# Optimization experiments

Measured on AMD Instinct MI355X. Metric: run time of the kernel, lower is better.

Reference implementation:

```python
import jax, jax.numpy as jnp
import numpy as np

B, D, HID, NB = 131072, 64, 256, 8
TAIL = 3.0
MIN_W = MIN_H = MIN_D = 1e-3
TR_IDX = np.arange(0, D, 2)  # mask > 0 -> transformed features (even indices)
ID_IDX = np.arange(1, D, 2)  # mask <= 0 -> identity features (odd indices)
DT = len(TR_IDX)


def _resnet(x, w_in, b_in, blocks, w_out, b_out):
    # nflows ResidualNet: initial linear, pre-activation residual blocks, final linear
    h = x @ w_in.T + b_in
    for (w0, b0, w1, b1) in blocks:
        t = jax.nn.relu(h)
        t = t @ w0.T + b0
        t = jax.nn.relu(t)
        t = t @ w1.T + b1
        h = h + t
    return h @ w_out.T + b_out


def _rq_spline(x, uw, uh, ud):
    # unconstrained rational-quadratic spline with linear tails (nflows)
    const = float(np.log(np.expm1(1.0 - MIN_D)))  # so softplus(const)+MIN_D == 1 at boundaries
    ud = jnp.pad(ud, ((0, 0), (0, 0), (1, 1)), constant_values=const)  # [B, DT, NB+1]
    inside = (x >= -TAIL) & (x <= TAIL)
    xc = jnp.clip(x, -TAIL, TAIL)

    widths = MIN_W + (1.0 - MIN_W * NB) * jax.nn.softmax(uw, axis=-1)
    cumw = jnp.pad(jnp.cumsum(widths, -1), ((0, 0), (0, 0), (1, 0)))
    cumw = 2.0 * TAIL * cumw - TAIL
    cumw = cumw.at[..., 0].set(-TAIL).at[..., -1].set(TAIL)
    widths = cumw[..., 1:] - cumw[..., :-1]

    heights = MIN_H + (1.0 - MIN_H * NB) * jax.nn.softmax(uh, axis=-1)
    cumh = jnp.pad(jnp.cumsum(heights, -1), ((0, 0), (0, 0), (1, 0)))
    cumh = 2.0 * TAIL * cumh - TAIL
    cumh = cumh.at[..., 0].set(-TAIL).at[..., -1].set(TAIL)
    heights = cumh[..., 1:] - cumh[..., :-1]

    deriv = MIN_D + jax.nn.softplus(ud)  # [B, DT, NB+1]

    # per-element bin search over cumulative widths
    idx = jnp.clip(jnp.sum((xc[..., None] >= cumw).astype(jnp.int32), -1) - 1, 0, NB - 1)[..., None]
    g = lambda t: jnp.take_along_axis(t, idx, axis=-1)[..., 0]

    in_cw, in_w = g(cumw[..., :-1]), g(widths)
    in_ch, in_h = g(cumh[..., :-1]), g(heights)
    in_delta = g(heights / widths)
    in_d, in_dp1 = g(deriv[..., :-1]), g(deriv[..., 1:])

    theta = (xc - in_cw) / in_w
    tom = theta * (1.0 - theta)
    num = in_h * (in_delta * theta * theta + in_d * tom)
    den = in_delta + (in_d + in_dp1 - 2.0 * in_delta) * tom
    y = in_ch + num / den
    dnum = in_delta * in_delta * (in_dp1 * theta * theta + 2.0 * in_delta * tom + in_d * (1.0 - theta) ** 2)
    lad = jnp.log(dnum) - 2.0 * jnp.log(den)
    return jnp.where(inside, y, x), jnp.where(inside, lad, 0.0)


def setup_inputs() -> dict:
    key = jax.random.key(0)
    ks = jax.random.split(key, 7)
    s_in = 1.0 / np.sqrt(DT)
    s_h = 1.0 / np.sqrt(HID)
    return {
        "inputs": jax.random.normal(ks[0], (B, D), jnp.float32),
        "w_in": jax.random.normal(ks[1], (HID, DT), jnp.float32) * s_in,
        "b_in": jnp.zeros((HID,), jnp.float32),
        "w0a": jax.random.normal(ks[2], (HID, HID), jnp.float32) * s_h,
        "b0a": jnp.zeros((HID,), jnp.float32),
        "w1a": jax.random.normal(ks[3], (HID, HID), jnp.float32) * s_h,
        "b1a": jnp.zeros((HID,), jnp.float32),
        "w0b": jax.random.normal(ks[4], (HID, HID), jnp.float32) * s_h,
        "b0b": jnp.zeros((HID,), jnp.float32),
        "w1b": jax.random.normal(ks[5], (HID, HID), jnp.float32) * s_h,
        "b1b": jnp.zeros((HID,), jnp.float32),
        "w_out": jax.random.normal(ks[6], (DT * (3 * NB - 1), HID), jnp.float32) * s_h,
        "b_out": jnp.zeros((DT * (3 * NB - 1),), jnp.float32),
    }


def reference(inputs, w_in, b_in, w0a, b0a, w1a, b1a, w0b, b0b, w1b, b1b, w_out, b_out):
    ident = inputs[:, ID_IDX]   # [B, DT]
    trans = inputs[:, TR_IDX]   # [B, DT]
    params = _resnet(ident, w_in, b_in, [(w0a, b0a, w1a, b1a), (w0b, b0b, w1b, b1b)], w_out, b_out)
    params = params.reshape(inputs.shape[0], DT, 3 * NB - 1)
    scale = 1.0 / np.sqrt(HID)  # module scales widths/heights by sqrt(hidden_features)
    uw = params[..., :NB] * scale
    uh = params[..., NB:2 * NB] * scale
    ud = params[..., 2 * NB:]
    y, lad = _rq_spline(trans, uw, uh, ud)
    out = jnp.zeros_like(inputs).at[:, ID_IDX].set(ident).at[:, TR_IDX].set(y)
    return out, jnp.sum(lad, axis=1)  # sum_except_batch
```

## Files before the change

### kernel.cpp

```cpp
#include <hip/hip_runtime.h>
#include <hip/hip_bf16.h>

#define B_TOTAL 131072
#define TS 264
#define PS 193

typedef short short8v __attribute__((ext_vector_type(8)));
typedef float f32x4 __attribute__((ext_vector_type(4)));

__device__ __forceinline__ unsigned short f2bf(float f) {
  union { float f; unsigned u; } v; v.f = f;
  unsigned r = v.u + 0x7FFFu + ((v.u >> 16) & 1u);
  return (unsigned short)(r >> 16);
}

__device__ __forceinline__ unsigned short f2bf_hw(float f) {
  __hip_bfloat16 h = __float2bfloat16(f);
  return *reinterpret_cast<unsigned short*>(&h);
}

__device__ __forceinline__ float frcp(float x) { return __builtin_amdgcn_rcpf(x); }

#define W_IN_OFF   0
#define W0A_OFF    8192
#define W1A_OFF    73728
#define W0B_OFF    139264
#define W1B_OFF    204800
#define WOUT_OFF   270336
#define WS_ELEMS   466944

__global__ void prep_weights(const float* __restrict__ w_in,
                             const float* __restrict__ w0a,
                             const float* __restrict__ w1a,
                             const float* __restrict__ w0b,
                             const float* __restrict__ w1b,
                             const float* __restrict__ w_out,
                             unsigned short* __restrict__ ws) {
  int idx = blockIdx.x * 256 + threadIdx.x;
  if (idx >= WS_ELEMS) return;
  float v;
  if (idx < W0A_OFF)       v = w_in[idx];
  else if (idx < W1A_OFF)  v = w0a[idx - W0A_OFF];
  else if (idx < W0B_OFF)  v = w1a[idx - W1A_OFF];
  else if (idx < W1B_OFF)  v = w0b[idx - W0B_OFF];
  else if (idx < WOUT_OFF) v = w1b[idx - W1B_OFF];
  else {
    int p = idx - WOUT_OFF;
    int row = p >> 8, k = p & 255;
    int dim = row / 24, j = row - dim * 24;
    v = (j < 23) ? w_out[(dim * 23 + j) * 256 + k] : 0.f;
  }
  ws[idx] = f2bf(v);
}

__global__ __launch_bounds__(256, 2)
void fused_main(const float* __restrict__ inp,
                const float* __restrict__ b_in,
                const float* __restrict__ b0a, const float* __restrict__ b1a,
                const float* __restrict__ b0b, const float* __restrict__ b1b,
                const float* __restrict__ b_out,
                const unsigned short* __restrict__ ws,
                float* __restrict__ outp) {
  __shared__ unsigned short Xs[64 * TS];
  __shared__ unsigned short Ys[64 * TS];

  const int tid  = threadIdx.x;
  const int lane = tid & 63;
  const int wave = tid >> 6;
  const int l15  = lane & 15;
  const int lhi  = lane >> 4;
  const int row0 = blockIdx.x * 64;

  const f32x4 zero4 = {0.f, 0.f, 0.f, 0.f};

  f32x4 hreg[4][4];

  {
#pragma unroll
    for (int mi = 0; mi < 4; mi++)
#pragma unroll
      for (int ni = 0; ni < 4; ni++) hreg[mi][ni] = zero4;

    short8v a[4];
#pragma unroll
    for (int mi = 0; mi < 4; mi++) {
      int rg = row0 + mi * 16 + l15;
      const float2* s2 = (const float2*)(inp + (long)rg * 64) + lhi * 8;
#pragma unroll
      for (int i = 0; i < 8; i++)
        a[mi][i] = (short)f2bf_hw(s2[i].y);
    }
    short8v b[4];
#pragma unroll
    for (int ni = 0; ni < 4; ni++) {
      int col = wave * 64 + ni * 16 + l15;
      b[ni] = *(const short8v*)(ws + W_IN_OFF + col * 32 + lhi * 8);
    }
#pragma unroll
    for (int mi = 0; mi < 4; mi++)
#pragma unroll
      for (int ni = 0; ni < 4; ni++)
        hreg[mi][ni] = __builtin_amdgcn_mfma_f32_16x16x32_bf16(a[mi], b[ni], hreg[mi][ni], 0, 0, 0);

#pragma unroll
    for (int ni = 0; ni < 4; ni++) {
      int col = wave * 64 + ni * 16 + l15;
      float bias = b_in[col];
#pragma unroll
      for (int mi = 0; mi < 4; mi++)
#pragma unroll
        for (int r = 0; r < 4; r++) {
          hreg[mi][ni][r] += bias;
          int rl = mi * 16 + lhi * 4 + r;
          Xs[rl * TS + col] = f2bf_hw(fmaxf(hreg[mi][ni][r], 0.f));
        }
    }
  }
  __syncthreads();

#pragma unroll
  for (int blk = 0; blk < 2; ++blk) {
    const unsigned short* wAp = ws + (blk == 0 ? W0A_OFF : W0B_OFF);
    const unsigned short* wBp = ws + (blk == 0 ? W1A_OFF : W1B_OFF);
    const float* bAp = (blk == 0) ? b0a : b0b;
    const float* bBp = (blk == 0) ? b1a : b1b;

    {
      f32x4 acc[4][4];
#pragma unroll
      for (int mi = 0; mi < 4; mi++)
#pragma unroll
        for (int ni = 0; ni < 4; ni++) acc[mi][ni] = zero4;

      for (int kk = 0; kk < 8; ++kk) {
        int kb = kk * 32 + lhi * 8;
        short8v a[4];
#pragma unroll
        for (int mi = 0; mi < 4; mi++)
          a[mi] = *(const short8v*)&Xs[(mi * 16 + l15) * TS + kb];
        short8v b[4];
#pragma unroll
        for (int ni = 0; ni < 4; ni++) {
          int col = wave * 64 + ni * 16 + l15;
          b[ni] = *(const short8v*)(wAp + col * 256 + kb);
        }
#pragma unroll
        for (int mi = 0; mi < 4; mi++)
#pragma unroll
          for (int ni = 0; ni < 4; ni++)
            acc[mi][ni] = __builtin_amdgcn_mfma_f32_16x16x32_bf16(a[mi], b[ni], acc[mi][ni], 0, 0, 0);
      }
#pragma unroll
      for (int ni = 0; ni < 4; ni++) {
        int col = wave * 64 + ni * 16 + l15;
        float bias = bAp[col];
#pragma unroll
        for (int mi = 0; mi < 4; mi++)
#pragma unroll
          for (int r = 0; r < 4; r++) {
            int rl = mi * 16 + lhi * 4 + r;
            Ys[rl * TS + col] = f2bf_hw(fmaxf(acc[mi][ni][r] + bias, 0.f));
          }
      }
    }
    __syncthreads();

    {
      f32x4 acc[4][4];
#pragma unroll
      for (int mi = 0; mi < 4; mi++)
#pragma unroll
        for (int ni = 0; ni < 4; ni++) acc[mi][ni] = zero4;

      for (int kk = 0; kk < 8; ++kk) {
        int kb = kk * 32 + lhi * 8;
        short8v a[4];
#pragma unroll
        for (int mi = 0; mi < 4; mi++)
          a[mi] = *(const short8v*)&Ys[(mi * 16 + l15) * TS + kb];
        short8v b[4];
#pragma unroll
        for (int ni = 0; ni < 4; ni++) {
          int col = wave * 64 + ni * 16 + l15;
          b[ni] = *(const short8v*)(wBp + col * 256 + kb);
        }
#pragma unroll
        for (int mi = 0; mi < 4; mi++)
#pragma unroll
          for (int ni = 0; ni < 4; ni++)
            acc[mi][ni] = __builtin_amdgcn_mfma_f32_16x16x32_bf16(a[mi], b[ni], acc[mi][ni], 0, 0, 0);
      }
#pragma unroll
      for (int ni = 0; ni < 4; ni++) {
        int col = wave * 64 + ni * 16 + l15;
        float bias = bBp[col];
#pragma unroll
        for (int mi = 0; mi < 4; mi++)
#pragma unroll
          for (int r = 0; r < 4; r++) {
            hreg[mi][ni][r] += acc[mi][ni][r] + bias;
            float hv = hreg[mi][ni][r];
            int rl = mi * 16 + lhi * 4 + r;
            Xs[rl * TS + col] = f2bf_hw(blk == 0 ? fmaxf(hv, 0.f) : hv);
          }
      }
    }
    __syncthreads();
  }

  float* p_lds = reinterpret_cast<float*>(Ys);

  float lad0 = 0.f, lad1 = 0.f;
  const int dl  = tid & 7;
  const int rsp = tid >> 3;

  for (int chunk = 0; chunk < 4; ++chunk) {
    f32x4 acc[4][3];
#pragma unroll
    for (int mi = 0; mi < 4; mi++)
#pragma unroll
      for (int ni = 0; ni < 3; ni++) acc[mi][ni] = zero4;

    for (int kk = 0; kk < 8; ++kk) {
      int kb = kk * 32 + lhi * 8;
      short8v a[4];
#pragma unroll
      for (int mi = 0; mi < 4; mi++)
        a[mi] = *(const short8v*)&Xs[(mi * 16 + l15) * TS + kb];
      short8v b[3];
#pragma unroll
      for (int ni = 0; ni < 3; ni++) {
        int col = chunk * 192 + wave * 48 + ni * 16 + l15;
        b[ni] = *(const short8v*)(ws + WOUT_OFF + col * 256 + kb);
      }
#pragma unroll
      for (int mi = 0; mi < 4; mi++)
#pragma unroll
        for (int ni = 0; ni < 3; ni++)
          acc[mi][ni] = __builtin_amdgcn_mfma_f32_16x16x32_bf16(a[mi], b[ni], acc[mi][ni], 0, 0, 0);
    }

#pragma unroll
    for (int half = 0; half < 2; ++half) {
#pragma unroll
      for (int ni = 0; ni < 3; ni++) {
        int cl = wave * 48 + ni * 16 + l15;
        int cg = chunk * 192 + cl;
        int dim = cg / 24;
        int j = cg - dim * 24;
        float bias = (j < 23) ? b_out[dim * 23 + j] : 0.f;
#pragma unroll
        for (int mi2 = 0; mi2 < 2; mi2++)
#pragma unroll
          for (int r = 0; r < 4; r++) {
            int rl = mi2 * 16 + lhi * 4 + r;
            if (j < 23)
              p_lds[rl * PS + cl] = acc[half * 2 + mi2][ni][r] + bias;
          }
      }
      __syncthreads();

      {
        const float S = 0.0625f;
        int dg = chunk * 8 + dl;
        int rg = row0 + half * 32 + rsp;
        const float* pb = &p_lds[rsp * PS + dl * 24];

        float2 xin = *(const float2*)(inp + (long)rg * 64 + 2 * dg);
        float x = xin.x, idv = xin.y;

        float pw[8], ph[8];
#pragma unroll
        for (int i = 0; i < 8; i++) { pw[i] = pb[i] * S; ph[i] = pb[8 + i] * S; }
        float mw = pw[0], mh = ph[0];
#pragma unroll
        for (int i = 1; i < 8; i++) { mw = fmaxf(mw, pw[i]); mh = fmaxf(mh, ph[i]); }
        float ew[8], eh[8], sw = 0.f, sh = 0.f;
#pragma unroll
        for (int i = 0; i < 8; i++) {
          ew[i] = __expf(pw[i] - mw); sw += ew[i];
          eh[i] = __expf(ph[i] - mh); sh += eh[i];
        }
        float invw = 0.992f * frcp(sw), invh = 0.992f * frcp(sh);

        float dv[9];
        dv[0] = 1.f; dv[8] = 1.f;
#pragma unroll
        for (int i = 1; i < 8; i++) {
          float u = pb[16 + i - 1];
          float sp = (u > 15.f) ? u : __logf(1.f + __expf(u));
          dv[i] = 0.001f + sp;
        }

        bool inside = (x >= -3.f) && (x <= 3.f);
        float xc = fminf(3.f, fmaxf(-3.f, x));

        float elo = -3.f, flo = -3.f, cw = 0.f, ch = 0.f;
        float in_cw = -3.f, in_w = 1.f, in_ch = -3.f, in_h = 1.f, in_d = 1.f, in_dp1 = 1.f;
#pragma unroll
        for (int i = 0; i < 8; i++) {
          float wi = 0.001f + ew[i] * invw; cw += wi;
          float hi = 0.001f + eh[i] * invh; ch += hi;
          float ehi = (i == 7) ? 3.f : 6.f * cw - 3.f;
          float fhi = (i == 7) ? 3.f : 6.f * ch - 3.f;
          bool take = (i == 0) || (xc >= elo);
          if (take) {
            in_cw = elo; in_w = ehi - elo;
            in_ch = flo; in_h = fhi - flo;
            in_d = dv[i]; in_dp1 = dv[i + 1];
          }
          elo = ehi; flo = fhi;
        }

        float rw   = frcp(in_w);
        float th   = (xc - in_cw) * rw;
        float omt  = 1.f - th;
        float tom  = th * omt;
        float delta = in_h * rw;
        float num  = in_h * (delta * th * th + in_d * tom);
        float den  = delta + (in_d + in_dp1 - 2.f * delta) * tom;
        float y    = in_ch + num * frcp(den);
        float dnum = delta * delta * (in_dp1 * th * th + 2.f * delta * tom + in_d * omt * omt);
        float lad  = __logf(dnum) - 2.f * __logf(den);

        float yout = inside ? y : x;
        float ladv = inside ? lad : 0.f;

        float2 o; o.x = yout; o.y = idv;
        *(float2*)(outp + (long)rg * 64 + 2 * dg) = o;

        if (half == 0) lad0 += ladv; else lad1 += ladv;
      }
      __syncthreads();
    }
  }

#pragma unroll
  for (int off = 1; off < 8; off <<= 1) {
    lad0 += __shfl_xor(lad0, off);
    lad1 += __shfl_xor(lad1, off);
  }
  if (dl == 0) {
    outp[(long)B_TOTAL * 64 + row0 + rsp]      = lad0;
    outp[(long)B_TOTAL * 64 + row0 + 32 + rsp] = lad1;
  }
}

extern "C" void kernel_launch(void* const* d_in, const int* in_sizes, int n_in,
                              void* d_out, int out_size, void* d_ws, size_t ws_size,
                              hipStream_t stream) {
  const float* inputs = (const float*)d_in[0];
  const float* w_in   = (const float*)d_in[1];
  const float* b_in   = (const float*)d_in[2];
  const float* w0a    = (const float*)d_in[3];
  const float* b0a    = (const float*)d_in[4];
  const float* w1a    = (const float*)d_in[5];
  const float* b1a    = (const float*)d_in[6];
  const float* w0b    = (const float*)d_in[7];
  const float* b0b    = (const float*)d_in[8];
  const float* w1b    = (const float*)d_in[9];
  const float* b1b    = (const float*)d_in[10];
  const float* w_out  = (const float*)d_in[11];
  const float* b_out  = (const float*)d_in[12];
  unsigned short* ws  = (unsigned short*)d_ws;
  float* outp = (float*)d_out;

  prep_weights<<<dim3((WS_ELEMS + 255) / 256), dim3(256), 0, stream>>>(
      w_in, w0a, w1a, w0b, w1b, w_out, ws);
  fused_main<<<dim3(2048), dim3(256), 0, stream>>>(
      inputs, b_in, b0a, b1a, b0b, b1b, b_out, ws, outp);
}
```

Baseline: 390.7 us.

## Swizzle LDS activation layout and software-pipeline GEMM operand loads

Replaces the padded row stride of 264 in the LDS activation tiles with an XOR-swizzled 256-wide layout, which is meant to avoid bank conflicts while trimming LDS use. It also moves the GEMM k-loops into helpers that fully unroll and prefetch operands: global weight fragments are loaded two steps ahead in a triple buffer, and LDS A fragments one step ahead in a double buffer. The goal is to hide global and LDS load latency behind the MFMA work. The extra buffering raises VGPR pressure under launch_bounds(256,2), which could cause spills or lower occupancy.

```diff
diff --git a/kernel.cpp b/kernel.cpp
--- a/kernel.cpp
+++ b/kernel.cpp
@@ -2,7 +2,6 @@
 #include <hip/hip_bf16.h>
 
 #define B_TOTAL 131072
-#define TS 264
 #define PS 193
 
 typedef short short8v __attribute__((ext_vector_type(8)));
@@ -20,6 +19,10 @@
 }
 
 __device__ __forceinline__ float frcp(float x) { return __builtin_amdgcn_rcpf(x); }
+
+__device__ __forceinline__ int swz(int row, int col) {
+  return row * 256 + (((col >> 3) ^ (row & 7)) << 3) + (col & 7);
+}
 
 #define W_IN_OFF   0
 #define W0A_OFF    8192
@@ -53,6 +56,68 @@
   ws[idx] = f2bf(v);
 }
 
+__device__ __forceinline__ void lda4(short8v a[4], const unsigned short* S,
+                                     int l15, int lhi, int kk) {
+  const int su = ((kk * 4 + lhi) ^ (l15 & 7)) << 3;
+#pragma unroll
+  for (int mi = 0; mi < 4; mi++)
+    a[mi] = *(const short8v*)&S[(mi * 16 + l15) * 256 + su];
+}
+
+__device__ __forceinline__ void ldb4(short8v b[4], const unsigned short* __restrict__ wP,
+                                     int cb, int l15, int lhi, int kk) {
+#pragma unroll
+  for (int ni = 0; ni < 4; ni++)
+    b[ni] = *(const short8v*)(wP + (cb + ni * 16 + l15) * 256 + kk * 32 + lhi * 8);
+}
+
+__device__ __forceinline__ void ldb3(short8v b[3], const unsigned short* __restrict__ wP,
+                                     int cb, int l15, int lhi, int kk) {
+#pragma unroll
+  for (int ni = 0; ni < 3; ni++)
+    b[ni] = *(const short8v*)(wP + (cb + ni * 16 + l15) * 256 + kk * 32 + lhi * 8);
+}
+
+__device__ __forceinline__ void mm4(f32x4 acc[4][4], const unsigned short* S,
+                                    const unsigned short* __restrict__ wP,
+                                    int cb, int l15, int lhi) {
+  short8v a[2][4], b[3][4];
+  lda4(a[0], S, l15, lhi, 0);
+  ldb4(b[0], wP, cb, l15, lhi, 0);
+  ldb4(b[1], wP, cb, l15, lhi, 1);
+#pragma unroll
+  for (int kk = 0; kk < 8; ++kk) {
+    if (kk < 6) ldb4(b[(kk + 2) % 3], wP, cb, l15, lhi, kk + 2);
+    if (kk < 7) lda4(a[(kk + 1) & 1], S, l15, lhi, kk + 1);
+#pragma unroll
+    for (int mi = 0; mi < 4; mi++)
+#pragma unroll
+      for (int ni = 0; ni < 4; ni++)
+        acc[mi][ni] = __builtin_amdgcn_mfma_f32_16x16x32_bf16(
+            a[kk & 1][mi], b[kk % 3][ni], acc[mi][ni], 0, 0, 0);
+  }
+}
+
+__device__ __forceinline__ void mm3(f32x4 acc[4][3], const unsigned short* S,
+                                    const unsigned short* __restrict__ wP,
+                                    int cb, int l15, int lhi) {
+  short8v a[2][4], b[3][3];
+  lda4(a[0], S, l15, lhi, 0);
+  ldb3(b[0], wP, cb, l15, lhi, 0);
+  ldb3(b[1], wP, cb, l15, lhi, 1);
+#pragma unroll
+  for (int kk = 0; kk < 8; ++kk) {
+    if (kk < 6) ldb3(b[(kk + 2) % 3], wP, cb, l15, lhi, kk + 2);
+    if (kk < 7) lda4(a[(kk + 1) & 1], S, l15, lhi, kk + 1);
+#pragma unroll
+    for (int mi = 0; mi < 4; mi++)
+#pragma unroll
+      for (int ni = 0; ni < 3; ni++)
+        acc[mi][ni] = __builtin_amdgcn_mfma_f32_16x16x32_bf16(
+            a[kk & 1][mi], b[kk % 3][ni], acc[mi][ni], 0, 0, 0);
+  }
+}
+
 __global__ __launch_bounds__(256, 2)
 void fused_main(const float* __restrict__ inp,
                 const float* __restrict__ b_in,
@@ -61,8 +126,8 @@
                 const float* __restrict__ b_out,
                 const unsigned short* __restrict__ ws,
                 float* __restrict__ outp) {
-  __shared__ unsigned short Xs[64 * TS];
-  __shared__ unsigned short Ys[64 * TS];
+  __shared__ unsigned short Xs[64 * 256];
+  __shared__ unsigned short Ys[64 * 256];
 
   const int tid  = threadIdx.x;
   const int lane = tid & 63;
@@ -112,7 +177,7 @@
         for (int r = 0; r < 4; r++) {
           hreg[mi][ni][r] += bias;
           int rl = mi * 16 + lhi * 4 + r;
-          Xs[rl * TS + col] = f2bf_hw(fmaxf(hreg[mi][ni][r], 0.f));
+          Xs[swz(rl, col)] = f2bf_hw(fmaxf(hreg[mi][ni][r], 0.f));
         }
     }
   }
@@ -132,24 +197,8 @@
 #pragma unroll
         for (int ni = 0; ni < 4; ni++) acc[mi][ni] = zero4;
 
-      for (int kk = 0; kk < 8; ++kk) {
-        int kb = kk * 32 + lhi * 8;
-        short8v a[4];
-#pragma unroll
-        for (int mi = 0; mi < 4; mi++)
-          a[mi] = *(const short8v*)&Xs[(mi * 16 + l15) * TS + kb];
-        short8v b[4];
-#pragma unroll
-        for (int ni = 0; ni < 4; ni++) {
-          int col = wave * 64 + ni * 16 + l15;
-          b[ni] = *(const short8v*)(wAp + col * 256 + kb);
-        }
-#pragma unroll
-        for (int mi = 0; mi < 4; mi++)
-#pragma unroll
-          for (int ni = 0; ni < 4; ni++)
-            acc[mi][ni] = __builtin_amdgcn_mfma_f32_16x16x32_bf16(a[mi], b[ni], acc[mi][ni], 0, 0, 0);
-      }
+      mm4(acc, Xs, wAp, wave * 64, l15, lhi);
+
 #pragma unroll
       for (int ni = 0; ni < 4; ni++) {
         int col = wave * 64 + ni * 16 + l15;
@@ -159,7 +208,7 @@
 #pragma unroll
           for (int r = 0; r < 4; r++) {
             int rl = mi * 16 + lhi * 4 + r;
-            Ys[rl * TS + col] = f2bf_hw(fmaxf(acc[mi][ni][r] + bias, 0.f));
+            Ys[swz(rl, col)] = f2bf_hw(fmaxf(acc[mi][ni][r] + bias, 0.f));
           }
       }
     }
@@ -172,24 +221,8 @@
 #pragma unroll
         for (int ni = 0; ni < 4; ni++) acc[mi][ni] = zero4;
 
-      for (int kk = 0; kk < 8; ++kk) {
-        int kb = kk * 32 + lhi * 8;
-        short8v a[4];
-#pragma unroll
-        for (int mi = 0; mi < 4; mi++)
-          a[mi] = *(const short8v*)&Ys[(mi * 16 + l15) * TS + kb];
-        short8v b[4];
-#pragma unroll
-        for (int ni = 0; ni < 4; ni++) {
-          int col = wave * 64 + ni * 16 + l15;
-          b[ni] = *(const short8v*)(wBp + col * 256 + kb);
-        }
-#pragma unroll
-        for (int mi = 0; mi < 4; mi++)
-#pragma unroll
-          for (int ni = 0; ni < 4; ni++)
-            acc[mi][ni] = __builtin_amdgcn_mfma_f32_16x16x32_bf16(a[mi], b[ni], acc[mi][ni], 0, 0, 0);
-      }
+      mm4(acc, Ys, wBp, wave * 64, l15, lhi);
+
 #pragma unroll
       for (int ni = 0; ni < 4; ni++) {
         int col = wave * 64 + ni * 16 + l15;
@@ -201,7 +234,7 @@
             hreg[mi][ni][r] += acc[mi][ni][r] + bias;
             float hv = hreg[mi][ni][r];
             int rl = mi * 16 + lhi * 4 + r;
-            Xs[rl * TS + col] = f2bf_hw(blk == 0 ? fmaxf(hv, 0.f) : hv);
+            Xs[swz(rl, col)] = f2bf_hw(blk == 0 ? fmaxf(hv, 0.f) : hv);
           }
       }
     }
@@ -221,24 +254,7 @@
 #pragma unroll
       for (int ni = 0; ni < 3; ni++) acc[mi][ni] = zero4;
 
-    for (int kk = 0; kk < 8; ++kk) {
-      int kb = kk * 32 + lhi * 8;
-      short8v a[4];
-#pragma unroll
-      for (int mi = 0; mi < 4; mi++)
-        a[mi] = *(const short8v*)&Xs[(mi * 16 + l15) * TS + kb];
-      short8v b[3];
-#pragma unroll
-      for (int ni = 0; ni < 3; ni++) {
-        int col = chunk * 192 + wave * 48 + ni * 16 + l15;
-        b[ni] = *(const short8v*)(ws + WOUT_OFF + col * 256 + kb);
-      }
-#pragma unroll
-      for (int mi = 0; mi < 4; mi++)
-#pragma unroll
-        for (int ni = 0; ni < 3; ni++)
-          acc[mi][ni] = __builtin_amdgcn_mfma_f32_16x16x32_bf16(a[mi], b[ni], acc[mi][ni], 0, 0, 0);
-    }
+    mm3(acc, Xs, ws + WOUT_OFF, chunk * 192 + wave * 48, l15, lhi);
 
 #pragma unroll
     for (int half = 0; half < 2; ++half) {
```

Result: no change. 397.9 us (+1.9%).

## Cut LDS footprint with swizzled single buffer and per-wave bf16 param staging

Applied to the files above, without the earlier changes.

The padded double activation buffers become a single XOR-swizzled 64x256 bf16 buffer, with extra barriers so it can be reused in place. Output-layer parameters are staged per wave in bf16 rather than in a shared fp32 tile, so the spline stage needs no block-wide barriers. The log-det reduction now runs through a small LDS array. The smaller LDS use allows raising the launch bound to 3 blocks per CU for more occupancy, but risks register spills and loses precision on the spline parameters.

```diff
diff --git a/kernel.cpp b/kernel.cpp
--- a/kernel.cpp
+++ b/kernel.cpp
@@ -2,8 +2,6 @@
 #include <hip/hip_bf16.h>
 
 #define B_TOTAL 131072
-#define TS 264
-#define PS 193
 
 typedef short short8v __attribute__((ext_vector_type(8)));
 typedef float f32x4 __attribute__((ext_vector_type(4)));
@@ -19,7 +17,15 @@
   return *reinterpret_cast<unsigned short*>(&h);
 }
 
+__device__ __forceinline__ float bf2f(unsigned short u) {
+  union { unsigned u; float f; } v; v.u = ((unsigned)u) << 16; return v.f;
+}
+
 __device__ __forceinline__ float frcp(float x) { return __builtin_amdgcn_rcpf(x); }
+
+__device__ __forceinline__ int swz(int row, int col) {
+  return row * 256 + (((col >> 3) ^ (row & 7)) << 3) + (col & 7);
+}
 
 #define W_IN_OFF   0
 #define W0A_OFF    8192
@@ -53,7 +59,7 @@
   ws[idx] = f2bf(v);
 }
 
-__global__ __launch_bounds__(256, 2)
+__global__ __launch_bounds__(256, 3)
 void fused_main(const float* __restrict__ inp,
                 const float* __restrict__ b_in,
                 const float* __restrict__ b0a, const float* __restrict__ b1a,
@@ -61,8 +67,9 @@
                 const float* __restrict__ b_out,
                 const unsigned short* __restrict__ ws,
                 float* __restrict__ outp) {
-  __shared__ unsigned short Xs[64 * TS];
-  __shared__ unsigned short Ys[64 * TS];
+  __shared__ unsigned short Xs[64 * 256];
+  __shared__ unsigned short Pstage[4 * 1536];
+  __shared__ float Red[256];
 
   const int tid  = threadIdx.x;
   const int lane = tid & 63;
@@ -112,7 +119,7 @@
         for (int r = 0; r < 4; r++) {
           hreg[mi][ni][r] += bias;
           int rl = mi * 16 + lhi * 4 + r;
-          Xs[rl * TS + col] = f2bf_hw(fmaxf(hreg[mi][ni][r], 0.f));
+          Xs[swz(rl, col)] = f2bf_hw(fmaxf(hreg[mi][ni][r], 0.f));
         }
     }
   }
@@ -133,23 +140,21 @@
         for (int ni = 0; ni < 4; ni++) acc[mi][ni] = zero4;
 
       for (int kk = 0; kk < 8; ++kk) {
-        int kb = kk * 32 + lhi * 8;
-        short8v a[4];
-#pragma unroll
-        for (int mi = 0; mi < 4; mi++)
-          a[mi] = *(const short8v*)&Xs[(mi * 16 + l15) * TS + kb];
-        short8v b[4];
-#pragma unroll
-        for (int ni = 0; ni < 4; ni++) {
-          int col = wave * 64 + ni * 16 + l15;
-          b[ni] = *(const short8v*)(wAp + col * 256 + kb);
-        }
+        const int su = ((kk * 4 + lhi) ^ (l15 & 7)) << 3;
+        short8v a[4], b[4];
+#pragma unroll
+        for (int mi = 0; mi < 4; mi++)
+          a[mi] = *(const short8v*)&Xs[(mi * 16 + l15) * 256 + su];
+#pragma unroll
+        for (int ni = 0; ni < 4; ni++)
+          b[ni] = *(const short8v*)(wAp + (wave * 64 + ni * 16 + l15) * 256 + kk * 32 + lhi * 8);
 #pragma unroll
         for (int mi = 0; mi < 4; mi++)
 #pragma unroll
           for (int ni = 0; ni < 4; ni++)
             acc[mi][ni] = __builtin_amdgcn_mfma_f32_16x16x32_bf16(a[mi], b[ni], acc[mi][ni], 0, 0, 0);
       }
+      __syncthreads();
 #pragma unroll
       for (int ni = 0; ni < 4; ni++) {
         int col = wave * 64 + ni * 16 + l15;
@@ -159,11 +164,11 @@
 #pragma unroll
           for (int r = 0; r < 4; r++) {
             int rl = mi * 16 + lhi * 4 + r;
-            Ys[rl * TS + col] = f2bf_hw(fmaxf(acc[mi][ni][r] + bias, 0.f));
+            Xs[swz(rl, col)] = f2bf_hw(fmaxf(acc[mi][ni][r] + bias, 0.f));
           }
       }
-    }
-    __syncthreads();
+      __syncthreads();
+    }
 
     {
       f32x4 acc[4][4];
@@ -173,23 +178,21 @@
         for (int ni = 0; ni < 4; ni++) acc[mi][ni] = zero4;
 
       for (int kk = 0; kk < 8; ++kk) {
-        int kb = kk * 32 + lhi * 8;
-        short8v a[4];
-#pragma unroll
-        for (int mi = 0; mi < 4; mi++)
-          a[mi] = *(const short8v*)&Ys[(mi * 16 + l15) * TS + kb];
-        short8v b[4];
-#pragma unroll
-        for (int ni = 0; ni < 4; ni++) {
-          int col = wave * 64 + ni * 16 + l15;
-          b[ni] = *(const short8v*)(wBp + col * 256 + kb);
-        }
+        const int su = ((kk * 4 + lhi) ^ (l15 & 7)) << 3;
+        short8v a[4], b[4];
+#pragma unroll
+        for (int mi = 0; mi < 4; mi++)
+          a[mi] = *(const short8v*)&Xs[(mi * 16 + l15) * 256 + su];
+#pragma unroll
+        for (int ni = 0; ni < 4; ni++)
+          b[ni] = *(const short8v*)(wBp + (wave * 64 + ni * 16 + l15) * 256 + kk * 32 + lhi * 8);
 #pragma unroll
         for (int mi = 0; mi < 4; mi++)
 #pragma unroll
           for (int ni = 0; ni < 4; ni++)
             acc[mi][ni] = __builtin_amdgcn_mfma_f32_16x16x32_bf16(a[mi], b[ni], acc[mi][ni], 0, 0, 0);
       }
+      __syncthreads();
 #pragma unroll
       for (int ni = 0; ni < 4; ni++) {
         int col = wave * 64 + ni * 16 + l15;
@@ -201,18 +204,17 @@
             hreg[mi][ni][r] += acc[mi][ni][r] + bias;
             float hv = hreg[mi][ni][r];
             int rl = mi * 16 + lhi * 4 + r;
-            Xs[rl * TS + col] = f2bf_hw(blk == 0 ? fmaxf(hv, 0.f) : hv);
+            Xs[swz(rl, col)] = f2bf_hw(blk == 0 ? fmaxf(hv, 0.f) : hv);
           }
       }
-    }
-    __syncthreads();
-  }
-
-  float* p_lds = reinterpret_cast<float*>(Ys);
+      __syncthreads();
+    }
+  }
 
   float lad0 = 0.f, lad1 = 0.f;
-  const int dl  = tid & 7;
-  const int rsp = tid >> 3;
+  const int dsl = lane >> 5;
+  const int rsp = lane & 31;
+  unsigned short* Pw = &Pstage[wave * 1536];
 
   for (int chunk = 0; chunk < 4; ++chunk) {
     f32x4 acc[4][3];
@@ -222,16 +224,15 @@
       for (int ni = 0; ni < 3; ni++) acc[mi][ni] = zero4;
 
     for (int kk = 0; kk < 8; ++kk) {
-      int kb = kk * 32 + lhi * 8;
-      short8v a[4];
-#pragma unroll
-      for (int mi = 0; mi < 4; mi++)
-        a[mi] = *(const short8v*)&Xs[(mi * 16 + l15) * TS + kb];
-      short8v b[3];
+      const int su = ((kk * 4 + lhi) ^ (l15 & 7)) << 3;
+      short8v a[4], b[3];
+#pragma unroll
+      for (int mi = 0; mi < 4; mi++)
+        a[mi] = *(const short8v*)&Xs[(mi * 16 + l15) * 256 + su];
 #pragma unroll
       for (int ni = 0; ni < 3; ni++) {
         int col = chunk * 192 + wave * 48 + ni * 16 + l15;
-        b[ni] = *(const short8v*)(ws + WOUT_OFF + col * 256 + kb);
+        b[ni] = *(const short8v*)(ws + WOUT_OFF + col * 256 + kk * 32 + lhi * 8);
       }
 #pragma unroll
       for (int mi = 0; mi < 4; mi++)
@@ -241,37 +242,46 @@
     }
 
 #pragma unroll
-    for (int half = 0; half < 2; ++half) {
+    for (int hf = 0; hf < 2; ++hf) {
 #pragma unroll
       for (int ni = 0; ni < 3; ni++) {
-        int cl = wave * 48 + ni * 16 + l15;
-        int cg = chunk * 192 + cl;
-        int dim = cg / 24;
-        int j = cg - dim * 24;
+        int cl = ni * 16 + l15;
+        int ds = (cl >= 24) ? 1 : 0;
+        int j  = cl - ds * 24;
+        int dim = chunk * 8 + wave * 2 + ds;
         float bias = (j < 23) ? b_out[dim * 23 + j] : 0.f;
 #pragma unroll
         for (int mi2 = 0; mi2 < 2; mi2++)
 #pragma unroll
           for (int r = 0; r < 4; r++) {
-            int rl = mi2 * 16 + lhi * 4 + r;
+            int row = mi2 * 16 + lhi * 4 + r;
             if (j < 23)
-              p_lds[rl * PS + cl] = acc[half * 2 + mi2][ni][r] + bias;
+              Pw[ds * 768 + row * 24 + j] = f2bf_hw(acc[hf * 2 + mi2][ni][r] + bias);
           }
       }
-      __syncthreads();
 
       {
         const float S = 0.0625f;
-        int dg = chunk * 8 + dl;
-        int rg = row0 + half * 32 + rsp;
-        const float* pb = &p_lds[rsp * PS + dl * 24];
+        int dg = chunk * 8 + wave * 2 + dsl;
+        int rg = row0 + hf * 32 + rsp;
+        const unsigned short* pb16 = &Pw[dsl * 768 + rsp * 24];
+        short8v pv0 = *(const short8v*)(pb16);
+        short8v pv1 = *(const short8v*)(pb16 + 8);
+        short8v pv2 = *(const short8v*)(pb16 + 16);
+        float pf[24];
+#pragma unroll
+        for (int i = 0; i < 8; i++) {
+          pf[i]      = bf2f((unsigned short)pv0[i]);
+          pf[8 + i]  = bf2f((unsigned short)pv1[i]);
+          pf[16 + i] = bf2f((unsigned short)pv2[i]);
+        }
 
         float2 xin = *(const float2*)(inp + (long)rg * 64 + 2 * dg);
         float x = xin.x, idv = xin.y;
 
         float pw[8], ph[8];
 #pragma unroll
-        for (int i = 0; i < 8; i++) { pw[i] = pb[i] * S; ph[i] = pb[8 + i] * S; }
+        for (int i = 0; i < 8; i++) { pw[i] = pf[i] * S; ph[i] = pf[8 + i] * S; }
         float mw = pw[0], mh = ph[0];
 #pragma unroll
         for (int i = 1; i < 8; i++) { mw = fmaxf(mw, pw[i]); mh = fmaxf(mh, ph[i]); }
@@ -287,7 +297,7 @@
         dv[0] = 1.f; dv[8] = 1.f;
 #pragma unroll
         for (int i = 1; i < 8; i++) {
-          float u = pb[16 + i - 1];
+          float u = pf[16 + i - 1];
           float sp = (u > 15.f) ? u : __logf(1.f + __expf(u));
           dv[i] = 0.001f + sp;
         }
@@ -329,20 +339,21 @@
         float2 o; o.x = yout; o.y = idv;
         *(float2*)(outp + (long)rg * 64 + 2 * dg) = o;
 
-        if (half == 0) lad0 += ladv; else lad1 += ladv;
-      }
-      __syncthreads();
-    }
-  }
-
-#pragma unroll
-  for (int off = 1; off < 8; off <<= 1) {
-    lad0 += __shfl_xor(lad0, off);
-    lad1 += __shfl_xor(lad1, off);
-  }
-  if (dl == 0) {
-    outp[(long)B_TOTAL * 64 + row0 + rsp]      = lad0;
-    outp[(long)B_TOTAL * 64 + row0 + 32 + rsp] = lad1;
+        if (hf == 0) lad0 += ladv; else lad1 += ladv;
+      }
+    }
+  }
+
+  lad0 += __shfl_xor(lad0, 32);
+  lad1 += __shfl_xor(lad1, 32);
+  if (lane < 32) {
+    Red[wave * 64 + lane]      = lad0;
+    Red[wave * 64 + 32 + lane] = lad1;
+  }
+  __syncthreads();
+  if (tid < 64) {
+    float s = Red[tid] + Red[64 + tid] + Red[128 + tid] + Red[192 + tid];
+    outp[(long)B_TOTAL * 64 + row0 + tid] = s;
   }
 }
 
```

New measurement: 627.2 us. +60.6%, slower.
